# Optimization experiments

Measured on AMD Instinct MI355X. Metric: run time of the kernel, lower is better.

## Reference

```python
import jax, jax.numpy as jnp
import numpy as np

NEG_BIG = -9e15
ALPHA = 0.2  # leaky relu slope


def setup_inputs() -> dict:
    key = jax.random.key(0)
    k_h, k_adj, k_W, k_a = jax.random.split(key, 4)
    N, F_in, F_out = 8192, 512, 64
    h = jax.random.normal(k_h, (N, F_in), dtype=jnp.float32)
    adj = jax.random.randint(k_adj, (N, N), 0, 2, dtype=jnp.int32)
    adj = adj.at[jnp.arange(N), jnp.arange(N)].set(1)  # self-loops (add_self_loops)
    # xavier_uniform with gain=1.414
    limW = 1.414 * np.sqrt(6.0 / (F_in + F_out))
    W = jax.random.uniform(k_W, (F_in, F_out), jnp.float32, -limW, limW)
    lima = 1.414 * np.sqrt(6.0 / (2 * F_out + 1))
    a = jax.random.uniform(k_a, (2 * F_out, 1), jnp.float32, -lima, lima)
    return {"h": h, "adj": adj, "W": W, "a": a}


def reference(h, adj, W, a):
    F_out = W.shape[1]
    Wh = h @ W                                  # [N, F_out]
    # a_input[i,j] = concat(Wh[i], Wh[j]); a_input @ a == Wh@a1 + (Wh@a2)^T
    a1, a2 = a[:F_out, 0], a[F_out:, 0]
    src = Wh @ a1                               # [N]
    dst = Wh @ a2                               # [N]
    e = jax.nn.leaky_relu(src[:, None] + dst[None, :], ALPHA)  # [N, N]
    att = jnp.where(adj > 0, e, NEG_BIG)
    att = jax.nn.softmax(att, axis=1)
    # dropout is identity in eval mode (training=False)
    return att @ Wh                             # [N, F_out]
```

## Files before the change

kernel.cpp:

```cpp
#include <hip/hip_runtime.h>
#include <hip/hip_bf16.h>

#define N 8192
#define FIN 512
#define FOUT 64
#define L2E 1.44269504089f
#define SPLIT 8

typedef __attribute__((address_space(1))) const void* gas_cptr;
typedef __attribute__((address_space(3))) void* las_ptr;
typedef float f32x4 __attribute__((ext_vector_type(4)));
typedef short bf16x8 __attribute__((ext_vector_type(8)));

#if __has_builtin(__builtin_amdgcn_exp2f)
#define EXP2(x) __builtin_amdgcn_exp2f(x)
#else
#define EXP2(x) exp2f(x)
#endif

static __device__ __forceinline__ unsigned short f2bf_rne(float f) {
  unsigned u = __float_as_uint(f);
  u += 0x7FFFu + ((u >> 16) & 1u);
  return (unsigned short)(u >> 16);
}
static __device__ __forceinline__ unsigned fkey(float f) {
  unsigned u = __float_as_uint(f);
  return (u & 0x80000000u) ? ~u : (u | 0x80000000u);
}

__global__ __launch_bounds__(256) void k_wh(
    const float* __restrict__ h, const float* __restrict__ W,
    const float* __restrict__ a, unsigned short* __restrict__ WhT,
    float* __restrict__ src2, float* __restrict__ dst2,
    unsigned* __restrict__ dmaxk) {
  __shared__ __attribute__((aligned(16))) char wts[64 * 512 * 2];
  __shared__ __attribute__((aligned(16))) char hsb[2][64 * 64 * 2];

  const int t = threadIdx.x;
  const int w = t >> 6;
  const int ll = t & 63;
  const int lc = ll & 15;
  const int row0 = blockIdx.x * 64;

  {
    const int k0 = t * 2;
#pragma unroll
    for (int f4 = 0; f4 < 16; ++f4) {
      float4 x0 = *reinterpret_cast<const float4*>(&W[(size_t)k0 * FOUT + f4 * 4]);
      float4 x1 = *reinterpret_cast<const float4*>(&W[(size_t)(k0 + 1) * FOUT + f4 * 4]);
      const float e0[4] = {x0.x, x0.y, x0.z, x0.w};
      const float e1[4] = {x1.x, x1.y, x1.z, x1.w};
#pragma unroll
      for (int e = 0; e < 4; ++e) {
        int f = f4 * 4 + e;
        int bb = f * 1024 + k0 * 2;
        bb ^= (f & 7) << 4;
        *reinterpret_cast<ushort2*>(wts + bb) =
            make_ushort2(f2bf_rne(e0[e]), f2bf_rne(e1[e]));
      }
    }
  }
  __syncthreads();

  f32x4 acc[4];
#pragma unroll
  for (int c = 0; c < 4; ++c) acc[c] = (f32x4){0.f, 0.f, 0.f, 0.f};

  const int hrow = 16 * w + (ll >> 2);
  const float* hbase = &h[(size_t)(row0 + hrow) * FIN + (ll & 3) * 16];

#define LOADH(dst, kc)                                                        \
  do {                                                                        \
    dst[0] = *reinterpret_cast<const float4*>(hbase + (kc));                  \
    dst[1] = *reinterpret_cast<const float4*>(hbase + (kc) + 4);              \
    dst[2] = *reinterpret_cast<const float4*>(hbase + (kc) + 8);              \
    dst[3] = *reinterpret_cast<const float4*>(hbase + (kc) + 12);             \
  } while (0)

#define WRITEH(buf, src)                                                      \
  do {                                                                        \
    int bb0 = hrow * 128 + (ll & 3) * 32;                                     \
    bb0 ^= (hrow & 7) << 4;                                                   \
    _Pragma("unroll") for (int q = 0; q < 4; ++q) {                           \
      ushort4 u = make_ushort4(f2bf_rne(src[q].x), f2bf_rne(src[q].y),        \
                               f2bf_rne(src[q].z), f2bf_rne(src[q].w));       \
      *reinterpret_cast<ushort4*>(hsb[buf] + (bb0 ^ (q * 8))) = u;            \
    }                                                                         \
  } while (0)

#define MFMA_CHUNK(buf, kcb)                                                  \
  do {                                                                        \
    _Pragma("unroll") for (int k0 = 0; k0 < 2; ++k0) {                        \
      int arow = 16 * w + lc;                                                 \
      int ab = arow * 128 + k0 * 64 + ((ll >> 4) << 4);                       \
      ab ^= (arow & 7) << 4;                                                  \
      bf16x8 af = *reinterpret_cast<const bf16x8*>(hsb[buf] + ab);            \
      _Pragma("unroll") for (int c = 0; c < 4; ++c) {                         \
        int f = c * 16 + lc;                                                  \
        int bb = f * 1024 + (kcb) + k0 * 64 + ((ll >> 4) << 4);               \
        bb ^= (f & 7) << 4;                                                   \
        bf16x8 bfr = *reinterpret_cast<const bf16x8*>(wts + bb);              \
        acc[c] = __builtin_amdgcn_mfma_f32_16x16x32_bf16(af, bfr, acc[c], 0, 0, 0); \
      }                                                                       \
    }                                                                         \
  } while (0)

  float4 ha[4], hb[4];
  LOADH(ha, 0);
#pragma unroll
  for (int c2 = 0; c2 < 4; ++c2) {
    WRITEH(0, ha);
    LOADH(hb, (2 * c2 + 1) * 64);
    MFMA_CHUNK(0, (2 * c2) * 128);
    WRITEH(1, hb);
    if (c2 < 3) LOADH(ha, (2 * c2 + 2) * 64);
    MFMA_CHUNK(1, (2 * c2 + 1) * 128);
  }

  float a1v[4], a2v[4];
#pragma unroll
  for (int c = 0; c < 4; ++c) {
    a1v[c] = a[c * 16 + lc];
    a2v[c] = a[FOUT + c * 16 + lc];
  }
  float p1[4], p2[4];
#pragma unroll
  for (int q = 0; q < 4; ++q) {
    p1[q] = acc[0][q] * a1v[0] + acc[1][q] * a1v[1] + acc[2][q] * a1v[2] + acc[3][q] * a1v[3];
    p2[q] = acc[0][q] * a2v[0] + acc[1][q] * a2v[1] + acc[2][q] * a2v[2] + acc[3][q] * a2v[3];
  }
#pragma unroll
  for (int msk = 8; msk >= 1; msk >>= 1)
#pragma unroll
    for (int q = 0; q < 4; ++q) {
      p1[q] += __shfl_xor(p1[q], msk);
      p2[q] += __shfl_xor(p2[q], msk);
    }
#pragma unroll
  for (int q = 0; q < 4; ++q) { p1[q] *= L2E; p2[q] *= L2E; }

  const int r0 = row0 + 16 * w + ((ll >> 4) << 2);
  if (lc == 0) {
#pragma unroll
    for (int q = 0; q < 4; ++q) { src2[r0 + q] = p1[q]; dst2[r0 + q] = p2[q]; }
  }
#pragma unroll
  for (int c = 0; c < 4; ++c) {
    ushort4 u = make_ushort4(f2bf_rne(acc[c][0]), f2bf_rne(acc[c][1]),
                             f2bf_rne(acc[c][2]), f2bf_rne(acc[c][3]));
    *reinterpret_cast<ushort4*>(&WhT[(size_t)(c * 16 + lc) * N + r0]) = u;
  }
  float wm = fmaxf(fmaxf(p2[0], p2[1]), fmaxf(p2[2], p2[3]));
  wm = fmaxf(wm, __shfl_xor(wm, 16));
  wm = fmaxf(wm, __shfl_xor(wm, 32));
  if (ll == 0) atomicMax(dmaxk, fkey(wm));
#undef LOADH
#undef WRITEH
#undef MFMA_CHUNK
}

__global__ __launch_bounds__(256) void k_attn(
    const int* __restrict__ adj, const unsigned short* __restrict__ WhT,
    const float* __restrict__ src2, const float* __restrict__ dst2,
    const unsigned* __restrict__ dmaxk, float* __restrict__ out,
    float* __restrict__ Opart, float* __restrict__ lpart, const int split) {
  __shared__ __attribute__((aligned(16))) char whs[2 * 8192];
  __shared__ __attribute__((aligned(16))) char pbs[8192];

  const int t = threadIdx.x;
  const int w = t >> 6;
  const int ll = t & 63;
  const int rg = t >> 4;
  const int cg = t & 15;
  const int i0 = rg * 4;
  const int row0 = blockIdx.x * 64;
  const int jlen = N / split;
  const int jbase = blockIdx.y * jlen;
  const int ntiles = jlen / 64;

  unsigned kk = dmaxk[0];
  const float dmax2 = (kk & 0x80000000u) ? __uint_as_float(kk & 0x7FFFFFFFu)
                                         : __uint_as_float(~kk);

  float s2v[4], m2[4], l[4];
#pragma unroll
  for (int r = 0; r < 4; ++r) {
    s2v[r] = src2[row0 + i0 + r];
    float x = s2v[r] + dmax2;
    m2[r] = fmaxf(x, 0.2f * x);
    l[r] = 0.f;
  }

  f32x4 acc[4];
#pragma unroll
  for (int c = 0; c < 4; ++c) acc[c] = (f32x4){0.f, 0.f, 0.f, 0.f};

#define STAGE_WHS(buf, j0)                                                    \
  do {                                                                        \
    _Pragma("unroll") for (int i_ = 0; i_ < 2; ++i_) {                        \
      int slot = t + i_ * 256;                                                \
      int b = slot * 16;                                                      \
      int u = b ^ (((b >> 7) & 7) << 4);                                      \
      int f_ = u >> 7;                                                        \
      int jl = (u & 127) >> 1;                                                \
      __builtin_amdgcn_global_load_lds(                                       \
          (gas_cptr)(WhT + (size_t)f_ * N + (j0) + jl),                       \
          (las_ptr)(whs + (buf)*8192 + b), 16, 0, 0);                         \
    }                                                                         \
  } while (0)

#define LOAD_ADJ(AV, DV, j0)                                                  \
  do {                                                                        \
    _Pragma("unroll") for (int r_ = 0; r_ < 4; ++r_) {                        \
      int4 x_ = *reinterpret_cast<const int4*>(                               \
          &adj[(size_t)(row0 + i0 + r_) * N + (j0) + cg * 4]);                \
      AV[r_][0] = x_.x; AV[r_][1] = x_.y; AV[r_][2] = x_.z; AV[r_][3] = x_.w; \
    }                                                                         \
    float4 d_ = *reinterpret_cast<const float4*>(&dst2[(j0) + cg * 4]);       \
    DV[0] = d_.x; DV[1] = d_.y; DV[2] = d_.z; DV[3] = d_.w;                   \
  } while (0)

  int av[4][4], nav[4][4];
  float dv[4], ndv[4];
  STAGE_WHS(0, jbase);
  LOAD_ADJ(av, dv, jbase);

  for (int jt = 0; jt < ntiles; ++jt) {
    const int cur = jt & 1;
    __syncthreads();

    if (jt + 1 < ntiles) {
      STAGE_WHS(cur ^ 1, jbase + (jt + 1) * 64);
      LOAD_ADJ(nav, ndv, jbase + (jt + 1) * 64);
    }

    float p[4][4];
#pragma unroll
    for (int r = 0; r < 4; ++r) {
#pragma unroll
      for (int jj = 0; jj < 4; ++jj) {
        float x = s2v[r] + dv[jj];
        float e2 = fmaxf(x, 0.2f * x);
        float pe = EXP2(e2 - m2[r]);
        pe = av[r][jj] > 0 ? pe : 0.f;
        p[r][jj] = pe;
        l[r] += pe;
      }
    }
#pragma unroll
    for (int r = 0; r < 4; ++r) {
      unsigned u0 = __float_as_uint(p[r][0]);
      unsigned u1 = __float_as_uint(p[r][1]);
      unsigned u2 = __float_as_uint(p[r][2]);
      unsigned u3 = __float_as_uint(p[r][3]);
      uint2 pk = make_uint2((u0 >> 16) | (u1 & 0xFFFF0000u),
                            (u2 >> 16) | (u3 & 0xFFFF0000u));
      int row = i0 + r;
      int ba = (row << 7) + (cg << 3);
      ba ^= (row & 7) << 4;
      *reinterpret_cast<uint2*>(pbs + ba) = pk;
    }

    {
      const int lc = ll & 15;
      const int g16 = (ll >> 4) << 4;
#pragma unroll
      for (int k0 = 0; k0 < 2; ++k0) {
        int arow = 16 * w + lc;
        int ab = (arow << 7) + k0 * 64 + g16;
        ab ^= (arow & 7) << 4;
        bf16x8 af = *reinterpret_cast<const bf16x8*>(pbs + ab);
#pragma unroll
        for (int c = 0; c < 4; ++c) {
          int brow = c * 16 + lc;
          int bb = (brow << 7) + k0 * 64 + g16;
          bb ^= (brow & 7) << 4;
          bf16x8 bfr = *reinterpret_cast<const bf16x8*>(whs + cur * 8192 + bb);
          acc[c] = __builtin_amdgcn_mfma_f32_16x16x32_bf16(af, bfr, acc[c], 0, 0, 0);
        }
      }
    }

    if (jt + 1 < ntiles) {
#pragma unroll
      for (int r = 0; r < 4; ++r) {
#pragma unroll
        for (int jj = 0; jj < 4; ++jj) av[r][jj] = nav[r][jj];
        dv[r] = ndv[r];
      }
    }
  }

#pragma unroll
  for (int msk = 8; msk >= 1; msk >>= 1)
#pragma unroll
    for (int r = 0; r < 4; ++r) l[r] += __shfl_xor(l[r], msk);

  const int orow = row0 + 16 * w + ((ll >> 4) << 2);
  const int ocol = ll & 15;
  if (split == 1) {
#pragma unroll
    for (int c = 0; c < 4; ++c)
#pragma unroll
      for (int q = 0; q < 4; ++q)
        out[(size_t)(orow + q) * FOUT + c * 16 + ocol] = acc[c][q] / l[q];
  } else {
    const int pb = blockIdx.y;
#pragma unroll
    for (int c = 0; c < 4; ++c)
#pragma unroll
      for (int q = 0; q < 4; ++q)
        Opart[((size_t)pb * N + orow + q) * FOUT + c * 16 + ocol] = acc[c][q];
    if (cg == 0) {
#pragma unroll
      for (int r = 0; r < 4; ++r)
        lpart[(size_t)pb * N + row0 + i0 + r] = l[r];
    }
  }
#undef STAGE_WHS
#undef LOAD_ADJ
}

__global__ __launch_bounds__(256) void k_combine(
    const float* __restrict__ Opart, const float* __restrict__ lpart,
    float* __restrict__ out, const int split) {
  int idx = blockIdx.x * 256 + threadIdx.x;
  int row = idx >> 6;
  float num = 0.f, den = 0.f;
  for (int k = 0; k < split; ++k) {
    num += Opart[(size_t)k * N * FOUT + idx];
    den += lpart[(size_t)k * N + row];
  }
  out[idx] = num / den;
}

extern "C" void kernel_launch(void* const* d_in, const int* in_sizes, int n_in,
                              void* d_out, int out_size, void* d_ws, size_t ws_size,
                              hipStream_t stream) {
  const float* h = (const float*)d_in[0];
  const int* adj = (const int*)d_in[1];
  const float* W = (const float*)d_in[2];
  const float* a = (const float*)d_in[3];
  float* out = (float*)d_out;

  unsigned short* WhT = (unsigned short*)d_ws;
  float* src2 = (float*)(WhT + (size_t)FOUT * N);
  float* dst2 = src2 + N;
  unsigned* dmaxk = (unsigned*)(dst2 + N);
  float* Opart = (float*)(dmaxk + 64);

  const size_t base_bytes = (size_t)FOUT * N * 2 + 2 * N * 4 + 256;
  int split = SPLIT;
  while (split > 1 &&
         base_bytes + (size_t)split * ((size_t)N * FOUT + N) * 4 > ws_size)
    split >>= 1;
  float* lpart = Opart + (size_t)split * N * FOUT;

  hipMemsetAsync(dmaxk, 0, 4, stream);
  k_wh<<<dim3(N / 64), 256, 0, stream>>>(h, W, a, WhT, src2, dst2, dmaxk);
  k_attn<<<dim3(N / 64, split), 256, 0, stream>>>(adj, WhT, src2, dst2, dmaxk,
                                                  out, Opart, lpart, split);
  if (split > 1)
    k_combine<<<dim3((N * FOUT) / 256), 256, 0, stream>>>(Opart, lpart, out, split);
}
```

Baseline: 107.1 us.

## Pack adjacency into bitmask in a prepass and raise split-K to 16

Adds a k_pack kernel that reads the int32 adjacency matrix once and uses wave ballots to write a 1-bit-per-edge mask. The attention kernel then reads 32-bit mask words instead of int4 adjacency vectors. The full 256 MB adjacency is still read once, so the prepass cannot remove the dominant traffic. It adds an extra launch plus a mask write and read, and split goes from 8 to 16, which adds more partial-result traffic and combine work.

```diff
diff --git a/kernel.cpp b/kernel.cpp
--- a/kernel.cpp
+++ b/kernel.cpp
@@ -4,8 +4,9 @@
 #define N 8192
 #define FIN 512
 #define FOUT 64
+#define NW 256
 #define L2E 1.44269504089f
-#define SPLIT 8
+#define SPLIT 16
 
 typedef __attribute__((address_space(1))) const void* gas_cptr;
 typedef __attribute__((address_space(3))) void* las_ptr;
@@ -26,6 +27,35 @@
 static __device__ __forceinline__ unsigned fkey(float f) {
   unsigned u = __float_as_uint(f);
   return (u & 0x80000000u) ? ~u : (u | 0x80000000u);
+}
+
+__global__ __launch_bounds__(256) void k_pack(
+    const int* __restrict__ adj, unsigned* __restrict__ mask) {
+  const int t = threadIdx.x;
+  const int w = t >> 6, ll = t & 63;
+  const int row = blockIdx.x * 2 + (w >> 1);
+  const int jbase = (w & 1) * (N / 2);
+  const int* arow = adj + (size_t)row * N + jbase;
+  unsigned* mrow = mask + (size_t)row * NW + (jbase >> 5);
+#pragma unroll 1
+  for (int it = 0; it < 64; it += 4) {
+    int x0 = arow[(it + 0) * 64 + ll];
+    int x1 = arow[(it + 1) * 64 + ll];
+    int x2 = arow[(it + 2) * 64 + ll];
+    int x3 = arow[(it + 3) * 64 + ll];
+    unsigned long long b0 = __ballot(x0 != 0);
+    unsigned long long b1 = __ballot(x1 != 0);
+    unsigned long long b2 = __ballot(x2 != 0);
+    unsigned long long b3 = __ballot(x3 != 0);
+    if (ll == 0) {
+      *reinterpret_cast<uint4*>(&mrow[it * 2]) =
+          make_uint4((unsigned)b0, (unsigned)(b0 >> 32),
+                     (unsigned)b1, (unsigned)(b1 >> 32));
+      *reinterpret_cast<uint4*>(&mrow[it * 2 + 4]) =
+          make_uint4((unsigned)b2, (unsigned)(b2 >> 32),
+                     (unsigned)b3, (unsigned)(b3 >> 32));
+    }
+  }
 }
 
 __global__ __launch_bounds__(256) void k_wh(
@@ -160,7 +190,7 @@
 }
 
 __global__ __launch_bounds__(256) void k_attn(
-    const int* __restrict__ adj, const unsigned short* __restrict__ WhT,
+    const unsigned* __restrict__ mask, const unsigned short* __restrict__ WhT,
     const float* __restrict__ src2, const float* __restrict__ dst2,
     const unsigned* __restrict__ dmaxk, float* __restrict__ out,
     float* __restrict__ Opart, float* __restrict__ lpart, const int split) {
@@ -209,21 +239,21 @@
     }                                                                         \
   } while (0)
 
-#define LOAD_ADJ(AV, DV, j0)                                                  \
-  do {                                                                        \
-    _Pragma("unroll") for (int r_ = 0; r_ < 4; ++r_) {                        \
-      int4 x_ = *reinterpret_cast<const int4*>(                               \
-          &adj[(size_t)(row0 + i0 + r_) * N + (j0) + cg * 4]);                \
-      AV[r_][0] = x_.x; AV[r_][1] = x_.y; AV[r_][2] = x_.z; AV[r_][3] = x_.w; \
-    }                                                                         \
+#define LOAD_MSK(MW, DV, j0)                                                  \
+  do {                                                                        \
+    int wi_ = ((j0) >> 5) + (cg >> 3);                                        \
+    _Pragma("unroll") for (int r_ = 0; r_ < 4; ++r_)                          \
+      MW[r_] = mask[(size_t)(row0 + i0 + r_) * NW + wi_];                     \
     float4 d_ = *reinterpret_cast<const float4*>(&dst2[(j0) + cg * 4]);       \
     DV[0] = d_.x; DV[1] = d_.y; DV[2] = d_.z; DV[3] = d_.w;                   \
   } while (0)
 
-  int av[4][4], nav[4][4];
+  unsigned mw[4], nmw[4];
   float dv[4], ndv[4];
   STAGE_WHS(0, jbase);
-  LOAD_ADJ(av, dv, jbase);
+  LOAD_MSK(mw, dv, jbase);
+
+  const int bsh = (cg & 7) * 4;
 
   for (int jt = 0; jt < ntiles; ++jt) {
     const int cur = jt & 1;
@@ -231,18 +261,19 @@
 
     if (jt + 1 < ntiles) {
       STAGE_WHS(cur ^ 1, jbase + (jt + 1) * 64);
-      LOAD_ADJ(nav, ndv, jbase + (jt + 1) * 64);
+      LOAD_MSK(nmw, ndv, jbase + (jt + 1) * 64);
     }
 
     float p[4][4];
 #pragma unroll
     for (int r = 0; r < 4; ++r) {
+      unsigned b = mw[r] >> bsh;
 #pragma unroll
       for (int jj = 0; jj < 4; ++jj) {
         float x = s2v[r] + dv[jj];
         float e2 = fmaxf(x, 0.2f * x);
         float pe = EXP2(e2 - m2[r]);
-        pe = av[r][jj] > 0 ? pe : 0.f;
+        pe = (b & (1u << jj)) ? pe : 0.f;
         p[r][jj] = pe;
         l[r] += pe;
       }
@@ -283,11 +314,7 @@
 
     if (jt + 1 < ntiles) {
 #pragma unroll
-      for (int r = 0; r < 4; ++r) {
-#pragma unroll
-        for (int jj = 0; jj < 4; ++jj) av[r][jj] = nav[r][jj];
-        dv[r] = ndv[r];
-      }
+      for (int r = 0; r < 4; ++r) { mw[r] = nmw[r]; dv[r] = ndv[r]; }
     }
   }
 
@@ -318,7 +345,7 @@
     }
   }
 #undef STAGE_WHS
-#undef LOAD_ADJ
+#undef LOAD_MSK
 }
 
 __global__ __launch_bounds__(256) void k_combine(
@@ -347,9 +374,11 @@
   float* src2 = (float*)(WhT + (size_t)FOUT * N);
   float* dst2 = src2 + N;
   unsigned* dmaxk = (unsigned*)(dst2 + N);
-  float* Opart = (float*)(dmaxk + 64);
-
-  const size_t base_bytes = (size_t)FOUT * N * 2 + 2 * N * 4 + 256;
+  unsigned* mask = dmaxk + 64;
+  float* Opart = (float*)(mask + (size_t)N * NW);
+
+  const size_t base_bytes = (size_t)FOUT * N * 2 + 2 * N * 4 + 256 +
+                            (size_t)N * NW * 4;
   int split = SPLIT;
   while (split > 1 &&
          base_bytes + (size_t)split * ((size_t)N * FOUT + N) * 4 > ws_size)
@@ -357,8 +386,9 @@
   float* lpart = Opart + (size_t)split * N * FOUT;
 
   hipMemsetAsync(dmaxk, 0, 4, stream);
+  k_pack<<<dim3(N / 2), 256, 0, stream>>>(adj, mask);
   k_wh<<<dim3(N / 64), 256, 0, stream>>>(h, W, a, WhT, src2, dst2, dmaxk);
-  k_attn<<<dim3(N / 64, split), 256, 0, stream>>>(adj, WhT, src2, dst2, dmaxk,
+  k_attn<<<dim3(N / 64, split), 256, 0, stream>>>(mask, WhT, src2, dst2, dmaxk,
                                                   out, Opart, lpart, split);
   if (split > 1)
     k_combine<<<dim3((N * FOUT) / 256), 256, 0, stream>>>(Opart, lpart, out, split);
```

New measurement: 119.2 us. 1.11x slower.

## Compress adjacency to LDS bitmasks via ballot and read WhT directly

Applied to the files above, without the earlier changes.

The attention kernel now reads each 1024-column chunk of the int32 adjacency rows with coalesced loads. It compresses them into per-row bitmasks with wave ballots stored in LDS, then runs the softmax/MFMA loop using mask bits instead of per-thread integer registers. WhT fragments are loaded directly from global memory rather than staged through double-buffered LDS, and the per-tile block barrier is dropped because each wave only consumes its own P rows. This is meant to cut barrier and LDS-staging overhead, but it gives up the overlap between the adjacency stream and the compute phase.

```diff
diff --git a/kernel.cpp b/kernel.cpp
--- a/kernel.cpp
+++ b/kernel.cpp
@@ -6,6 +6,7 @@
 #define FOUT 64
 #define L2E 1.44269504089f
 #define SPLIT 8
+#define MSTRIDE 34
 
 typedef __attribute__((address_space(1))) const void* gas_cptr;
 typedef __attribute__((address_space(3))) void* las_ptr;
@@ -164,7 +165,7 @@
     const float* __restrict__ src2, const float* __restrict__ dst2,
     const unsigned* __restrict__ dmaxk, float* __restrict__ out,
     float* __restrict__ Opart, float* __restrict__ lpart, const int split) {
-  __shared__ __attribute__((aligned(16))) char whs[2 * 8192];
+  __shared__ unsigned mskd[64 * MSTRIDE];
   __shared__ __attribute__((aligned(16))) char pbs[8192];
 
   const int t = threadIdx.x;
@@ -173,10 +174,12 @@
   const int rg = t >> 4;
   const int cg = t & 15;
   const int i0 = rg * 4;
+  const int lc = ll & 15;
+  const int g16 = (ll >> 4) << 4;
+  const int g8 = (ll >> 4) << 3;
   const int row0 = blockIdx.x * 64;
   const int jlen = N / split;
   const int jbase = blockIdx.y * jlen;
-  const int ntiles = jlen / 64;
 
   unsigned kk = dmaxk[0];
   const float dmax2 = (kk & 0x80000000u) ? __uint_as_float(kk & 0x7FFFFFFFu)
@@ -195,75 +198,88 @@
 #pragma unroll
   for (int c = 0; c < 4; ++c) acc[c] = (f32x4){0.f, 0.f, 0.f, 0.f};
 
-#define STAGE_WHS(buf, j0)                                                    \
-  do {                                                                        \
-    _Pragma("unroll") for (int i_ = 0; i_ < 2; ++i_) {                        \
-      int slot = t + i_ * 256;                                                \
-      int b = slot * 16;                                                      \
-      int u = b ^ (((b >> 7) & 7) << 4);                                      \
-      int f_ = u >> 7;                                                        \
-      int jl = (u & 127) >> 1;                                                \
-      __builtin_amdgcn_global_load_lds(                                       \
-          (gas_cptr)(WhT + (size_t)f_ * N + (j0) + jl),                       \
-          (las_ptr)(whs + (buf)*8192 + b), 16, 0, 0);                         \
-    }                                                                         \
-  } while (0)
-
-#define LOAD_ADJ(AV, DV, j0)                                                  \
-  do {                                                                        \
-    _Pragma("unroll") for (int r_ = 0; r_ < 4; ++r_) {                        \
-      int4 x_ = *reinterpret_cast<const int4*>(                               \
-          &adj[(size_t)(row0 + i0 + r_) * N + (j0) + cg * 4]);                \
-      AV[r_][0] = x_.x; AV[r_][1] = x_.y; AV[r_][2] = x_.z; AV[r_][3] = x_.w; \
-    }                                                                         \
-    float4 d_ = *reinterpret_cast<const float4*>(&dst2[(j0) + cg * 4]);       \
-    DV[0] = d_.x; DV[1] = d_.y; DV[2] = d_.z; DV[3] = d_.w;                   \
-  } while (0)
-
-  int av[4][4], nav[4][4];
-  float dv[4], ndv[4];
-  STAGE_WHS(0, jbase);
-  LOAD_ADJ(av, dv, jbase);
-
-  for (int jt = 0; jt < ntiles; ++jt) {
-    const int cur = jt & 1;
+  const int bsh = (cg & 7) * 4;
+
+  for (int mt = 0; mt < jlen; mt += 1024) {
+    const int mbase = jbase + mt;
+
+#pragma unroll 1
+    for (int s = 0; s < 16; ++s) {
+      const int row = 16 * w + s;
+      const int* ar = adj + (size_t)(row0 + row) * N + mbase;
+      unsigned x[16];
+#pragma unroll
+      for (int k = 0; k < 16; ++k) x[k] = ar[k * 64 + ll];
+      unsigned long long b[16];
+#pragma unroll
+      for (int k = 0; k < 16; ++k) b[k] = __ballot(x[k] != 0);
+      if (ll == 0) {
+        unsigned long long* mrow =
+            reinterpret_cast<unsigned long long*>(&mskd[row * MSTRIDE]);
+#pragma unroll
+        for (int k = 0; k < 16; ++k) mrow[k] = b[k];
+      }
+    }
     __syncthreads();
 
-    if (jt + 1 < ntiles) {
-      STAGE_WHS(cur ^ 1, jbase + (jt + 1) * 64);
-      LOAD_ADJ(nav, ndv, jbase + (jt + 1) * 64);
-    }
-
-    float p[4][4];
-#pragma unroll
-    for (int r = 0; r < 4; ++r) {
-#pragma unroll
-      for (int jj = 0; jj < 4; ++jj) {
-        float x = s2v[r] + dv[jj];
-        float e2 = fmaxf(x, 0.2f * x);
-        float pe = EXP2(e2 - m2[r]);
-        pe = av[r][jj] > 0 ? pe : 0.f;
-        p[r][jj] = pe;
-        l[r] += pe;
-      }
-    }
-#pragma unroll
-    for (int r = 0; r < 4; ++r) {
-      unsigned u0 = __float_as_uint(p[r][0]);
-      unsigned u1 = __float_as_uint(p[r][1]);
-      unsigned u2 = __float_as_uint(p[r][2]);
-      unsigned u3 = __float_as_uint(p[r][3]);
-      uint2 pk = make_uint2((u0 >> 16) | (u1 & 0xFFFF0000u),
-                            (u2 >> 16) | (u3 & 0xFFFF0000u));
-      int row = i0 + r;
-      int ba = (row << 7) + (cg << 3);
-      ba ^= (row & 7) << 4;
-      *reinterpret_cast<uint2*>(pbs + ba) = pk;
-    }
-
+    unsigned mw[4], nmw[4];
+    float dv[4], ndv[4];
+#pragma unroll
+    for (int r = 0; r < 4; ++r)
+      mw[r] = mskd[(i0 + r) * MSTRIDE + (cg >> 3)];
     {
-      const int lc = ll & 15;
-      const int g16 = (ll >> 4) << 4;
+      float4 d_ = *reinterpret_cast<const float4*>(&dst2[mbase + cg * 4]);
+      dv[0] = d_.x; dv[1] = d_.y; dv[2] = d_.z; dv[3] = d_.w;
+    }
+
+#pragma unroll 1
+    for (int jt2 = 0; jt2 < 16; ++jt2) {
+      const int j0 = mbase + jt2 * 64;
+
+      bf16x8 bfr[2][4];
+#pragma unroll
+      for (int k0 = 0; k0 < 2; ++k0)
+#pragma unroll
+        for (int c = 0; c < 4; ++c)
+          bfr[k0][c] = *reinterpret_cast<const bf16x8*>(
+              &WhT[(size_t)(c * 16 + lc) * N + j0 + k0 * 32 + g8]);
+
+      if (jt2 + 1 < 16) {
+#pragma unroll
+        for (int r = 0; r < 4; ++r)
+          nmw[r] = mskd[(i0 + r) * MSTRIDE + (jt2 + 1) * 2 + (cg >> 3)];
+        float4 d_ = *reinterpret_cast<const float4*>(&dst2[j0 + 64 + cg * 4]);
+        ndv[0] = d_.x; ndv[1] = d_.y; ndv[2] = d_.z; ndv[3] = d_.w;
+      }
+
+      float p[4][4];
+#pragma unroll
+      for (int r = 0; r < 4; ++r) {
+        unsigned b = mw[r] >> bsh;
+#pragma unroll
+        for (int jj = 0; jj < 4; ++jj) {
+          float x = s2v[r] + dv[jj];
+          float e2 = fmaxf(x, 0.2f * x);
+          float pe = EXP2(e2 - m2[r]);
+          pe = (b & (1u << jj)) ? pe : 0.f;
+          p[r][jj] = pe;
+          l[r] += pe;
+        }
+      }
+#pragma unroll
+      for (int r = 0; r < 4; ++r) {
+        unsigned u0 = __float_as_uint(p[r][0]);
+        unsigned u1 = __float_as_uint(p[r][1]);
+        unsigned u2 = __float_as_uint(p[r][2]);
+        unsigned u3 = __float_as_uint(p[r][3]);
+        uint2 pk = make_uint2((u0 >> 16) | (u1 & 0xFFFF0000u),
+                              (u2 >> 16) | (u3 & 0xFFFF0000u));
+        int row = i0 + r;
+        int ba = (row << 7) + (cg << 3);
+        ba ^= (row & 7) << 4;
+        *reinterpret_cast<uint2*>(pbs + ba) = pk;
+      }
+
 #pragma unroll
       for (int k0 = 0; k0 < 2; ++k0) {
         int arow = 16 * w + lc;
@@ -271,24 +287,18 @@
         ab ^= (arow & 7) << 4;
         bf16x8 af = *reinterpret_cast<const bf16x8*>(pbs + ab);
 #pragma unroll
-        for (int c = 0; c < 4; ++c) {
-          int brow = c * 16 + lc;
-          int bb = (brow << 7) + k0 * 64 + g16;
-          bb ^= (brow & 7) << 4;
-          bf16x8 bfr = *reinterpret_cast<const bf16x8*>(whs + cur * 8192 + bb);
-          acc[c] = __builtin_amdgcn_mfma_f32_16x16x32_bf16(af, bfr, acc[c], 0, 0, 0);
-        }
-      }
-    }
-
-    if (jt + 1 < ntiles) {
-#pragma unroll
-      for (int r = 0; r < 4; ++r) {
-#pragma unroll
-        for (int jj = 0; jj < 4; ++jj) av[r][jj] = nav[r][jj];
-        dv[r] = ndv[r];
-      }
-    }
+        for (int c = 0; c < 4; ++c)
+          acc[c] = __builtin_amdgcn_mfma_f32_16x16x32_bf16(af, bfr[k0][c],
+                                                           acc[c], 0, 0, 0);
+      }
+
+      if (jt2 + 1 < 16) {
+#pragma unroll
+        for (int r = 0; r < 4; ++r) { mw[r] = nmw[r]; dv[r] = ndv[r]; }
+      }
+    }
+
+    if (mt + 1024 < jlen) __syncthreads();
   }
 
 #pragma unroll
@@ -317,8 +327,6 @@
         lpart[(size_t)pb * N + row0 + i0 + r] = l[r];
     }
   }
-#undef STAGE_WHS
-#undef LOAD_ADJ
 }
 
 __global__ __launch_bounds__(256) void k_combine(
```

After: 130.6 us. +21.9%, slower.
